# Kernel optimization log

Hardware: AMD Instinct MI355X
Metric: run time of the kernel (lower is better)

## Reference

```python
import jax, jax.numpy as jnp
import numpy as np

B, T, D = 128, 2048, 256


def setup_inputs() -> dict:
    key = jax.random.key(0)
    ks = jax.random.split(key, 6)
    s = 1.0 / np.sqrt(D)  # kaiming-uniform-ish scale for bias-free Linear
    return {
        "x": jax.random.normal(ks[0], (B, T, D), jnp.float32),
        "W_in": jax.random.normal(ks[1], (D, D), jnp.float32) * s,
        "W_select": jax.random.normal(ks[2], (D, D), jnp.float32) * s,
        "W_gate": jax.random.normal(ks[3], (D, D), jnp.float32) * s,
        "W_out": jax.random.normal(ks[4], (D, D), jnp.float32) * s,
        "W_delta": jax.random.normal(ks[5], (D, D), jnp.float32) * s,
        "log_a": jnp.zeros((D,), jnp.float32),  # module inits log_a = zeros
    }


def _diag_recurrence(decay, update):
    # state_t = decay_t * state_{t-1} + update_t, state_{-1} = 0 (zero-init fast path)
    # First-order linear recurrence as an associative scan:
    # (a1,b1) o (a2,b2) = (a1*a2, a2*b1 + b2)
    def combine(c1, c2):
        a1, b1 = c1
        a2, b2 = c2
        return a1 * a2, a2 * b1 + b2

    _, states = jax.lax.associative_scan(combine, (decay, update), axis=1)
    return states  # (B, T, D)


def reference(x, W_in, W_select, W_gate, W_out, W_delta, log_a):
    # selective diag-SSM (a_mode='diag'):
    #   delta  = softplus(delta_proj(x))                  timestep / selectivity
    #   decay  = exp(-delta * exp(log_a))                 in (0, 1]
    #   update = delta * sigmoid(select_proj(x)) * in_proj(x)
    #   states = scan(state = decay*state + update)
    #   y      = states * silu(gate_proj(x)); out = out_proj(y)
    delta = jax.nn.softplus(jnp.einsum("btd,ed->bte", x, W_delta))
    decay = jnp.exp(-delta * jnp.exp(log_a))
    u = jnp.einsum("btd,ed->bte", x, W_in)
    sel = jax.nn.sigmoid(jnp.einsum("btd,ed->bte", x, W_select))
    update = delta * sel * u
    states = _diag_recurrence(decay, update)
    gate = jax.nn.silu(jnp.einsum("btd,ed->bte", x, W_gate))
    return jnp.einsum("btd,ed->bte", states * gate, W_out)
```

## Files before the change

### kernel.cpp

```cpp
#include <hip/hip_runtime.h>
#include <hip/hip_bf16.h>
#include <hip/hip_fp16.h>
#include <math.h>


typedef __attribute__((ext_vector_type(8))) short s16x8;
typedef __attribute__((ext_vector_type(4))) float f32x4;

#define D_DIM 256
#define T_DIM 2048
#define B_DIM 128
#define NCHUNK2 32
#define CLEN 128
#define BK 64

__device__ __forceinline__ unsigned short f2bf(float f) {
    union { float f; unsigned int u; } v; v.f = f;
    unsigned int r = v.u + 0x7fffu + ((v.u >> 16) & 1u);
    return (unsigned short)(r >> 16);
}
__device__ __forceinline__ float bf2f(unsigned short s) {
    union { unsigned int u; float f; } v; v.u = ((unsigned int)s) << 16;
    return v.f;
}
__device__ __forceinline__ void gload_lds16(const void* g, void* l) {
    __builtin_amdgcn_global_load_lds(
        (const __attribute__((address_space(1))) unsigned int*)g,
        (__attribute__((address_space(3))) unsigned int*)l, 16, 0, 0);
}

__global__ __launch_bounds__(256) void prep_kernel(
    const float* __restrict__ W_in, const float* __restrict__ W_select,
    const float* __restrict__ W_gate, const float* __restrict__ W_out,
    const float* __restrict__ W_delta, const float* __restrict__ log_a,
    unsigned short* __restrict__ Wb, float* __restrict__ ea)
{
    int i = blockIdx.x * 256 + threadIdx.x;
    if (i < 4 * 65536) {
        int row = i >> 8, k = i & 255;
        int n = row >> 2, w = row & 3;
        const float* src = (w == 0) ? W_delta : (w == 1) ? W_select
                         : (w == 2) ? W_in    : W_gate;
        Wb[i] = f2bf(src[n * 256 + k]);
    } else if (i < 5 * 65536) {
        Wb[i] = f2bf(W_out[i - 4 * 65536]);
    } else if (i < 5 * 65536 + 256) {
        int j = i - 5 * 65536;
        ea[j] = expf(log_a[j]);
    }
}

__global__ __launch_bounds__(256) void xcast_kernel(
    const float* __restrict__ x, unsigned short* __restrict__ xb)
{
    size_t i = ((size_t)blockIdx.x * 256 + threadIdx.x) * 8;
    float4 p0 = *(const float4*)(x + i);
    float4 p1 = *(const float4*)(x + i + 4);
    s16x8 a;
    a[0] = (short)f2bf(p0.x); a[1] = (short)f2bf(p0.y);
    a[2] = (short)f2bf(p0.z); a[3] = (short)f2bf(p0.w);
    a[4] = (short)f2bf(p1.x); a[5] = (short)f2bf(p1.y);
    a[6] = (short)f2bf(p1.z); a[7] = (short)f2bf(p1.w);
    *(s16x8*)(xb + i) = a;
}

__global__ __launch_bounds__(256, 3) void gemm_fused_kernel(
    const unsigned short* __restrict__ xb, const unsigned short* __restrict__ Wcat,
    const float* __restrict__ ea,
    __half2* __restrict__ du, unsigned short* __restrict__ gate,
    float* __restrict__ cA, float* __restrict__ cS)
{
    __shared__ char lds[32768];
    int bid = blockIdx.x;
    int wg  = (bid & 7) * 2048 + (bid >> 3);
    int mt  = wg >> 3;
    int nt  = wg & 7;
    int mbase = mt * 128;
    int nb = nt * 128;
    int tid = threadIdx.x, lane = tid & 63, wid = tid >> 6;
    int l16 = lane & 15, lk = lane >> 4;
    int wr = wid >> 1, wc = wid & 1;
    int srow = tid >> 3;
    int sgi  = tid & 7;

    f32x4 acc[4][4] = {};

    for (int ks = 0; ks < 4; ++ks) {
        int kb = ks * BK;
#pragma unroll
        for (int j = 0; j < 4; ++j) {
            int row = j * 32 + srow;
            int sg  = sgi ^ (row & 7);
            gload_lds16(xb + (size_t)(mbase + row) * D_DIM + kb + sg * 8,
                        lds + row * 128 + sgi * 16);
        }
#pragma unroll
        for (int j = 0; j < 4; ++j) {
            int row = j * 32 + srow;
            int sg  = sgi ^ (row & 7);
            gload_lds16(Wcat + (size_t)(nb + row) * D_DIM + kb + sg * 8,
                        lds + 16384 + row * 128 + sgi * 16);
        }
        __syncthreads();

#pragma unroll
        for (int kk = 0; kk < 2; ++kk) {
            int gp = ((kk * 4 + lk) ^ (l16 & 7)) * 16;
            s16x8 xf[4], wf[4];
#pragma unroll
            for (int mf = 0; mf < 4; ++mf)
                xf[mf] = *(const s16x8*)(lds
                           + (wr * 64 + mf * 16 + l16) * 128 + gp);
#pragma unroll
            for (int nf = 0; nf < 4; ++nf)
                wf[nf] = *(const s16x8*)(lds + 16384
                           + (wc * 64 + nf * 16 + l16) * 128 + gp);
#pragma unroll
            for (int nf = 0; nf < 4; ++nf)
#pragma unroll
                for (int mf = 0; mf < 4; ++mf)
                    acc[mf][nf] = __builtin_amdgcn_mfma_f32_16x16x32_bf16(
                        wf[nf], xf[mf], acc[mf][nf], 0, 0, 0);
        }
        if (ks < 3) __syncthreads();
    }

#pragma unroll
    for (int nf = 0; nf < 4; ++nf) {
        int n = nt * 32 + wc * 16 + nf * 4 + lk;
        float ean = ea[n];
        float A[4], S[4];
#pragma unroll
        for (int mf = 0; mf < 4; ++mf) {
            int m = mbase + wr * 64 + mf * 16 + l16;
            float zd = acc[mf][nf][0];
            float zs = acc[mf][nf][1];
            float zi = acc[mf][nf][2];
            float zg = acc[mf][nf][3];
            float e = __expf(zd);
            float delta = (zd > 15.f) ? zd : __logf(1.f + e);
            float dec = __expf(-delta * ean);
            float sel = 1.f / (1.f + __expf(-zs));
            float upd = delta * sel * zi;
            float g   = zg / (1.f + __expf(-zg));
            du[(size_t)m * D_DIM + n] = __floats2half2_rn(dec, upd);
            gate[(size_t)m * D_DIM + n] = f2bf(g);
            A[mf] = dec;
            S[mf] = upd;
        }
#pragma unroll
        for (int d = 1; d < 16; d <<= 1) {
            bool upper = (l16 & d);
#pragma unroll
            for (int mf = 0; mf < 4; ++mf) {
                float Ap = __shfl_xor(A[mf], d, 64);
                float Sp = __shfl_xor(S[mf], d, 64);
                float Se = upper ? Sp : S[mf];
                float Al = upper ? A[mf] : Ap;
                float Sl = upper ? S[mf] : Sp;
                S[mf] = fmaf(Al, Se, Sl);
                A[mf] = A[mf] * Ap;
            }
        }
        float cAe = A[0], cSe = S[0];
#pragma unroll
        for (int mf = 1; mf < 4; ++mf) {
            cSe = fmaf(A[mf], cSe, S[mf]);
            cAe *= A[mf];
        }
        if (l16 == 0) {
            int hc = mt * 2 + wr;
            cA[hc * D_DIM + n] = cAe;
            cS[hc * D_DIM + n] = cSe;
        }
    }
}

__global__ __launch_bounds__(256) void scan2_kernel(
    const float* __restrict__ cA, const float* __restrict__ cS,
    float* __restrict__ carry)
{
    int b = blockIdx.x;
    int d = threadIdx.x;
    float s = 0.f;
    for (int c = 0; c < NCHUNK2; ++c) {
        int idx = (b * NCHUNK2 + c) * D_DIM + d;
        carry[idx] = s;
        s = fmaf(cA[idx], s, cS[idx]);
    }
}

__global__ __launch_bounds__(256) void scan_out_kernel(
    const __half2* __restrict__ du, const unsigned short* __restrict__ gate,
    const float* __restrict__ carry, const unsigned short* __restrict__ Wo,
    float* __restrict__ out)
{
    __shared__ unsigned short yls[128 * 256];
    int b = blockIdx.x >> 4;
    int c = blockIdx.x & 15;
    int tid = threadIdx.x;

    {
        int d = tid;
        size_t base = ((size_t)b * T_DIM + (size_t)c * CLEN) * D_DIM + d;
        float s = carry[(b * NCHUNK2 + c * 2) * D_DIM + d];
        int dlo = d & 7, dch = d >> 3;
#pragma unroll 4
        for (int t = 0; t < CLEN; ++t) {
            __half2 v = du[base + (size_t)t * D_DIM];
            float dc = __low2float(v);
            float up = __high2float(v);
            s = fmaf(dc, s, up);
            float g = bf2f(gate[base + (size_t)t * D_DIM]);
            int off = t * 256 + ((dch ^ (t & 7)) << 3) + dlo;
            yls[off] = f2bf(s * g);
        }
    }
    __syncthreads();

    int lane = tid & 63, wid = tid >> 6;
    int l16 = lane & 15;
    int lkc = lane >> 4;
    int m0 = (wid >> 1) * 64;
    size_t rbase = (size_t)b * T_DIM + (size_t)c * CLEN;
    int r0 = lkc * 4;

    for (int nblk = 0; nblk < 2; ++nblk) {
        int n0 = (wid & 1) * 64 + nblk * 128;
        f32x4 acc[4][4] = {};
        for (int ks = 0; ks < 8; ++ks) {
            int kb = ks * 32 + lkc * 8;
            s16x8 yf[4];
#pragma unroll
            for (int mf = 0; mf < 4; ++mf) {
                int row = m0 + mf * 16 + l16;
                int chunk = (ks * 4 + lkc) ^ (row & 7);
                yf[mf] = *(const s16x8*)&yls[row * 256 + chunk * 8];
            }
#pragma unroll
            for (int nf = 0; nf < 4; ++nf) {
                s16x8 wfr = *(const s16x8*)(Wo + (size_t)(n0 + nf * 16 + l16) * D_DIM + kb);
#pragma unroll
                for (int mf = 0; mf < 4; ++mf)
                    acc[mf][nf] = __builtin_amdgcn_mfma_f32_16x16x32_bf16(
                        wfr, yf[mf], acc[mf][nf], 0, 0, 0);
            }
        }
#pragma unroll
        for (int mf = 0; mf < 4; ++mf) {
            size_t rowg = rbase + m0 + mf * 16 + l16;
#pragma unroll
            for (int nf = 0; nf < 4; ++nf) {
                int n = n0 + nf * 16 + r0;
                *(f32x4*)(out + rowg * D_DIM + n) = acc[mf][nf];
            }
        }
    }
}

extern "C" void kernel_launch(void* const* d_in, const int* in_sizes, int n_in,
                              void* d_out, int out_size, void* d_ws, size_t ws_size,
                              hipStream_t stream)
{
    const float* x        = (const float*)d_in[0];
    const float* W_in     = (const float*)d_in[1];
    const float* W_select = (const float*)d_in[2];
    const float* W_gate   = (const float*)d_in[3];
    const float* W_out    = (const float*)d_in[4];
    const float* W_delta  = (const float*)d_in[5];
    const float* log_a    = (const float*)d_in[6];
    float* out = (float*)d_out;

    char* ws = (char*)d_ws;
    const size_t MB = 1ull << 20;
    unsigned short* Wb    = (unsigned short*)(ws);
    float*          ea    = (float*)(ws + 655360);
    unsigned short* xb    = (unsigned short*)(ws + 1 * MB);
    __half2*        du    = (__half2*)(ws + 129 * MB);
    unsigned short* gate  = (unsigned short*)(ws + 385 * MB);
    float*          cA    = (float*)(ws + 513 * MB);
    float*          cS    = (float*)(ws + 517 * MB);
    float*          carry = (float*)(ws + 521 * MB);

    prep_kernel<<<1281, 256, 0, stream>>>(W_in, W_select, W_gate, W_out,
                                          W_delta, log_a, Wb, ea);
    xcast_kernel<<<32768, 256, 0, stream>>>(x, xb);
    gemm_fused_kernel<<<16384, 256, 0, stream>>>(xb, Wb, ea, du, gate, cA, cS);
    scan2_kernel<<<B_DIM, 256, 0, stream>>>(cA, cS, carry);
    scan_out_kernel<<<B_DIM * NCHUNK2 / 2, 256, 0, stream>>>(du, gate, carry,
                                                             Wb + 4 * 65536, out);
}
```

Baseline: 647.3 us.

## Double-buffer GEMM K-loop with 32-wide stages and hand-placed waitcnt barriers

The fused projection GEMM used to load 64-wide K slices into one LDS buffer and sync before each compute. It now splits K into 32-wide slices across two 16 KB LDS buffers, prefetching the next slice while MFMAs run on the current one, with explicit vmcnt/lgkmcnt waits and sched barriers. The XOR swizzle changes to suit the 64-byte rows, and the ea loads move before the loop. This aims to hide global-to-LDS latency, at the cost of more barriers per K step and reliance on hand-tuned wait counts.

```diff
diff --git a/kernel.cpp b/kernel.cpp
--- a/kernel.cpp
+++ b/kernel.cpp
@@ -12,7 +12,6 @@
 #define B_DIM 128
 #define NCHUNK2 32
 #define CLEN 128
-#define BK 64
 
 __device__ __forceinline__ unsigned short f2bf(float f) {
     union { float f; unsigned int u; } v; v.f = f;
@@ -80,55 +79,94 @@
     int tid = threadIdx.x, lane = tid & 63, wid = tid >> 6;
     int l16 = lane & 15, lk = lane >> 4;
     int wr = wid >> 1, wc = wid & 1;
-    int srow = tid >> 3;
-    int sgi  = tid & 7;
+
+    const unsigned short* xg  = xb   + (size_t)mbase * D_DIM;
+    const unsigned short* wgp = Wcat + (size_t)nb * D_DIM;
+
+    int se0 = tid, se1 = 256 + tid;
+    int sr0 = se0 >> 2, sg0 = (se0 & 3) ^ ((sr0 >> 1) & 3);
+    int sr1 = se1 >> 2, sg1 = (se1 & 3) ^ ((sr1 >> 1) & 3);
+
+    float eav[4];
+#pragma unroll
+    for (int nf = 0; nf < 4; ++nf)
+        eav[nf] = ea[nt * 32 + wc * 16 + nf * 4 + lk];
+    asm volatile("s_waitcnt vmcnt(0)" ::: "memory");
+    __builtin_amdgcn_sched_barrier(0);
+
+#define STAGE(BUFB, KB)                                                     \
+    {                                                                        \
+        gload_lds16(xg  + (size_t)sr0 * D_DIM + (KB) + sg0 * 8,              \
+                    lds + (BUFB) + se0 * 16);                                \
+        gload_lds16(xg  + (size_t)sr1 * D_DIM + (KB) + sg1 * 8,              \
+                    lds + (BUFB) + se1 * 16);                                \
+        gload_lds16(wgp + (size_t)sr0 * D_DIM + (KB) + sg0 * 8,              \
+                    lds + (BUFB) + 8192 + se0 * 16);                         \
+        gload_lds16(wgp + (size_t)sr1 * D_DIM + (KB) + sg1 * 8,              \
+                    lds + (BUFB) + 8192 + se1 * 16);                         \
+    }
 
     f32x4 acc[4][4] = {};
 
-    for (int ks = 0; ks < 4; ++ks) {
-        int kb = ks * BK;
-#pragma unroll
-        for (int j = 0; j < 4; ++j) {
-            int row = j * 32 + srow;
-            int sg  = sgi ^ (row & 7);
-            gload_lds16(xb + (size_t)(mbase + row) * D_DIM + kb + sg * 8,
-                        lds + row * 128 + sgi * 16);
-        }
-#pragma unroll
-        for (int j = 0; j < 4; ++j) {
-            int row = j * 32 + srow;
-            int sg  = sgi ^ (row & 7);
-            gload_lds16(Wcat + (size_t)(nb + row) * D_DIM + kb + sg * 8,
-                        lds + 16384 + row * 128 + sgi * 16);
-        }
-        __syncthreads();
-
-#pragma unroll
-        for (int kk = 0; kk < 2; ++kk) {
-            int gp = ((kk * 4 + lk) ^ (l16 & 7)) * 16;
-            s16x8 xf[4], wf[4];
-#pragma unroll
-            for (int mf = 0; mf < 4; ++mf)
-                xf[mf] = *(const s16x8*)(lds
-                           + (wr * 64 + mf * 16 + l16) * 128 + gp);
-#pragma unroll
-            for (int nf = 0; nf < 4; ++nf)
-                wf[nf] = *(const s16x8*)(lds + 16384
-                           + (wc * 64 + nf * 16 + l16) * 128 + gp);
-#pragma unroll
-            for (int nf = 0; nf < 4; ++nf)
-#pragma unroll
-                for (int mf = 0; mf < 4; ++mf)
-                    acc[mf][nf] = __builtin_amdgcn_mfma_f32_16x16x32_bf16(
-                        wf[nf], xf[mf], acc[mf][nf], 0, 0, 0);
-        }
-        if (ks < 3) __syncthreads();
-    }
+#define COMPUTE(BUFB)                                                        \
+    {                                                                        \
+        s16x8 xf[4], wf[4];                                                  \
+        _Pragma("unroll")                                                    \
+        for (int mf = 0; mf < 4; ++mf) {                                     \
+            int row = wr * 64 + mf * 16 + l16;                               \
+            int g = lk ^ ((row >> 1) & 3);                                   \
+            xf[mf] = *(const s16x8*)(lds + (BUFB) + row * 64 + g * 16);      \
+        }                                                                    \
+        _Pragma("unroll")                                                    \
+        for (int nf = 0; nf < 4; ++nf) {                                     \
+            int row = wc * 64 + nf * 16 + l16;                               \
+            int g = lk ^ ((row >> 1) & 3);                                   \
+            wf[nf] = *(const s16x8*)(lds + (BUFB) + 8192 + row * 64 + g * 16);\
+        }                                                                    \
+        _Pragma("unroll")                                                    \
+        for (int nf = 0; nf < 4; ++nf)                                       \
+            _Pragma("unroll")                                                \
+            for (int mf = 0; mf < 4; ++mf)                                   \
+                acc[mf][nf] = __builtin_amdgcn_mfma_f32_16x16x32_bf16(       \
+                    wf[nf], xf[mf], acc[mf][nf], 0, 0, 0);                   \
+    }
+
+    STAGE(0, 0);
+#pragma unroll 1
+    for (int p = 0; p < 4; ++p) {
+        STAGE(16384, (2 * p + 1) * 32);
+        __builtin_amdgcn_sched_barrier(0);
+        asm volatile("s_waitcnt vmcnt(4)" ::: "memory");
+        __builtin_amdgcn_s_barrier();
+        __builtin_amdgcn_sched_barrier(0);
+        COMPUTE(0);
+        __builtin_amdgcn_sched_barrier(0);
+        asm volatile("s_waitcnt lgkmcnt(0)" ::: "memory");
+        __builtin_amdgcn_s_barrier();
+        __builtin_amdgcn_sched_barrier(0);
+        if (p < 3) {
+            STAGE(0, (2 * p + 2) * 32);
+            __builtin_amdgcn_sched_barrier(0);
+            asm volatile("s_waitcnt vmcnt(4)" ::: "memory");
+        } else {
+            __builtin_amdgcn_sched_barrier(0);
+            asm volatile("s_waitcnt vmcnt(0)" ::: "memory");
+        }
+        __builtin_amdgcn_s_barrier();
+        __builtin_amdgcn_sched_barrier(0);
+        COMPUTE(16384);
+        __builtin_amdgcn_sched_barrier(0);
+        asm volatile("s_waitcnt lgkmcnt(0)" ::: "memory");
+        __builtin_amdgcn_s_barrier();
+        __builtin_amdgcn_sched_barrier(0);
+    }
+#undef STAGE
+#undef COMPUTE
 
 #pragma unroll
     for (int nf = 0; nf < 4; ++nf) {
         int n = nt * 32 + wc * 16 + nf * 4 + lk;
-        float ean = ea[n];
+        float ean = eav[nf];
         float A[4], S[4];
 #pragma unroll
         for (int mf = 0; mf < 4; ++mf) {
```

Result: slower. 674.6 us (+4.2%).
